# Kernel tuning notes

Hardware: AMD Instinct MI355X
Metric: run time of the kernel (lower is better)

## Reference

```python
import jax, jax.numpy as jnp
import numpy as np

B, M, S = 4, 1024, 1024
D, H, FF = 1024, 16, 4096
NE, P = 128, 1
HD = D // H
EPS = 1e-5


def _layer_norm(x, g, b):
    mu = x.mean(-1, keepdims=True)
    var = ((x - mu) ** 2).mean(-1, keepdims=True)
    return (x - mu) * jax.lax.rsqrt(var + EPS) * g + b


def _mha(q_in, kv_in, in_w, in_b, out_w, out_b):
    # torch nn.MultiheadAttention: packed in_proj_weight [3D, D], y = x @ W.T + b
    wq, wk, wv = in_w[:D], in_w[D:2 * D], in_w[2 * D:]
    bq, bk, bv = in_b[:D], in_b[D:2 * D], in_b[2 * D:]
    q = (q_in @ wq.T + bq).reshape(q_in.shape[0], q_in.shape[1], H, HD)
    k = (kv_in @ wk.T + bk).reshape(kv_in.shape[0], kv_in.shape[1], H, HD)
    v = (kv_in @ wv.T + bv).reshape(kv_in.shape[0], kv_in.shape[1], H, HD)
    scores = jnp.einsum('bqhd,bkhd->bhqk', q, k) / jnp.sqrt(jnp.float32(HD))
    attn = jax.nn.softmax(scores, axis=-1)
    o = jnp.einsum('bhqk,bkhd->bqhd', attn, v).reshape(q_in.shape[0], q_in.shape[1], D)
    return o @ out_w.T + out_b


def _soft_moe(h, phi, exp_w, exp_b):
    # h: [b, m, FF]; phi: [FF, n, p]
    logits = jnp.einsum('bmd,dnp->bmnp', h, phi)
    dispatch = jax.nn.softmax(logits, axis=1)  # over tokens m
    b, m, n, p = logits.shape
    combine = jax.nn.softmax(logits.reshape(b, m, n * p), axis=-1).reshape(b, m, n, p)
    slots = jnp.einsum('bmd,bmnp->bnpd', h, dispatch)  # [b, n, p, FF]
    y = jnp.einsum('bnpd,ndo->bnpo', slots, exp_w) + exp_b[None, :, None, :]  # [b, n, p, D]
    return jnp.einsum('bnpo,bmnp->bmo', y, combine)


def setup_inputs() -> dict:
    key = jax.random.key(0)
    ks = jax.random.split(key, 16)
    sc = 0.02

    def rn(k, shape):
        return jax.random.normal(k, shape, jnp.float32) * sc

    return {
        'tgt': jax.random.normal(ks[0], (B, M, D), jnp.float32),
        'memory': jax.random.normal(ks[1], (B, S, D), jnp.float32),
        'sa_in_w': rn(ks[2], (3 * D, D)), 'sa_in_b': jnp.zeros((3 * D,), jnp.float32),
        'sa_out_w': rn(ks[3], (D, D)), 'sa_out_b': jnp.zeros((D,), jnp.float32),
        'ca_in_w': rn(ks[4], (3 * D, D)), 'ca_in_b': jnp.zeros((3 * D,), jnp.float32),
        'ca_out_w': rn(ks[5], (D, D)), 'ca_out_b': jnp.zeros((D,), jnp.float32),
        'norm1_g': jnp.ones((D,), jnp.float32), 'norm1_b': jnp.zeros((D,), jnp.float32),
        'norm2_g': jnp.ones((D,), jnp.float32), 'norm2_b': jnp.zeros((D,), jnp.float32),
        'norm3_g': jnp.ones((D,), jnp.float32), 'norm3_b': jnp.zeros((D,), jnp.float32),
        'lin_w': rn(ks[6], (FF, D)), 'lin_b': jnp.zeros((FF,), jnp.float32),
        'phi': rn(ks[7], (FF, NE, P)),
        'exp_w': rn(ks[8], (NE, FF, D)), 'exp_b': jnp.zeros((NE, D), jnp.float32),
    }


def reference(tgt, memory, sa_in_w, sa_in_b, sa_out_w, sa_out_b,
              ca_in_w, ca_in_b, ca_out_w, ca_out_b,
              norm1_g, norm1_b, norm2_g, norm2_b, norm3_g, norm3_b,
              lin_w, lin_b, phi, exp_w, exp_b):
    # post-norm (norm_first=False), dropout=0 (eval)
    x = tgt
    x = _layer_norm(x + _mha(x, x, sa_in_w, sa_in_b, sa_out_w, sa_out_b), norm1_g, norm1_b)
    x = _layer_norm(x + _mha(x, memory, ca_in_w, ca_in_b, ca_out_w, ca_out_b), norm2_g, norm2_b)
    h = jax.nn.relu(x @ lin_w.T + lin_b)  # [B, M, FF]
    ff = _soft_moe(h, phi, exp_w, exp_b)  # [B, M, D]
    x = _layer_norm(x + ff, norm3_g, norm3_b)
    return x
```

## Files before the change

kernel.cpp:

```cpp
#include <hip/hip_runtime.h>
#include <cstdint>
#include <cstddef>

typedef unsigned short u16;
typedef unsigned int   u32;
typedef short bf16x8 __attribute__((ext_vector_type(8)));
typedef float f32x4  __attribute__((ext_vector_type(4)));
typedef u16   u16x8  __attribute__((ext_vector_type(8)));
typedef u16   u16x4  __attribute__((ext_vector_type(4)));
typedef u16   u16x2  __attribute__((ext_vector_type(2)));

constexpr int B_  = 4;
constexpr int M_  = 1024;
constexpr int S_  = 1024;
constexpr int D_  = 1024;
constexpr int H_  = 16;
constexpr int FF_ = 4096;
constexpr int NE_ = 128;

__device__ __forceinline__ u16 f2bf(float f) {
    u32 u = __builtin_bit_cast(u32, f);
    u = (u + 0x7fffu + ((u >> 16) & 1u)) >> 16;
    return (u16)u;
}
__device__ __forceinline__ float bf2f(u16 u) {
    u32 x = ((u32)u) << 16;
    return __builtin_bit_cast(float, x);
}
__device__ __forceinline__ void gload_lds16(const u16* g, u16* l) {
    __builtin_amdgcn_global_load_lds(
        (const __attribute__((address_space(1))) u32*)g,
        (__attribute__((address_space(3))) u32*)l, 16, 0, 0);
}

template<int RELU>
__global__ __launch_bounds__(512, 1) void gemm256_mfma(
    const u16* __restrict__ A, const u16* __restrict__ W,
    const float* __restrict__ bias, u16* __restrict__ C,
    int K, int N, int lda, int ldw)
{
    __shared__ u16 lds[49152];
    const int tid = threadIdx.x;
    const int w = tid >> 6, l = tid & 63;
    const int wr = w >> 2, wc = w & 3;
    const int fr = l & 15, g = l >> 4;
    const int bm = blockIdx.y * 256, bn = blockIdx.x * 256;

    const int qcol = (((l & 3) ^ ((l >> 3) & 3))) * 8;
    const int srow = w * 16 + (l >> 2);
    const u16* aG0 = A + (size_t)(bm + srow) * lda + qcol;
    const u16* aG1 = aG0 + (size_t)128 * lda;
    const u16* bG0 = W + (size_t)(bn + srow) * ldw + qcol;
    const u16* bG1 = bG0 + (size_t)128 * ldw;
    const int wofs = w * 512;

    const int qsw = (g ^ ((fr >> 1) & 3)) * 8;
    const int aoff = (wr * 128 + fr) * 32 + qsw;
    const int boff = (wc * 64 + fr) * 32 + qsw;

    f32x4 acc[8][4];
#pragma unroll
    for (int i = 0; i < 8; ++i)
#pragma unroll
        for (int j = 0; j < 4; ++j)
#pragma unroll
            for (int q = 0; q < 4; ++q) acc[i][j][q] = 0.f;

    gload_lds16(aG0, &lds[0 + wofs]);
    gload_lds16(aG1, &lds[4096 + wofs]);
    gload_lds16(bG0, &lds[24576 + wofs]);
    gload_lds16(bG1, &lds[24576 + 4096 + wofs]);
    aG0 += 32; aG1 += 32; bG0 += 32; bG1 += 32;
    gload_lds16(aG0, &lds[8192 + wofs]);
    gload_lds16(aG1, &lds[8192 + 4096 + wofs]);
    gload_lds16(bG0, &lds[32768 + wofs]);
    gload_lds16(bG1, &lds[32768 + 4096 + wofs]);
    aG0 += 32; aG1 += 32; bG0 += 32; bG1 += 32;
    asm volatile("s_waitcnt vmcnt(4)" ::: "memory");
    __builtin_amdgcn_s_barrier();
    __builtin_amdgcn_sched_barrier(0);

    int rb = 0;

#define G256_STEP(ISSUE_, VMOPT_)                                            \
  {                                                                          \
    const int wb_ = (rb >= 1) ? rb - 1 : 2;                                  \
    const u16* Ab_ = &lds[rb * 8192];                                        \
    const u16* Bb_ = &lds[24576 + rb * 8192];                                \
    u16* Aw_ = &lds[wb_ * 8192];                                             \
    u16* Bw_ = &lds[24576 + wb_ * 8192];                                     \
    bf16x8 af_[4], bf_[4];                                                   \
    _Pragma("unroll") for (int mf = 0; mf < 4; ++mf)                         \
      af_[mf] = *(const bf16x8*)(Ab_ + aoff + mf * 512);                     \
    _Pragma("unroll") for (int nf = 0; nf < 4; ++nf)                         \
      bf_[nf] = *(const bf16x8*)(Bb_ + boff + nf * 512);                     \
    if (ISSUE_) {                                                            \
      gload_lds16(aG0, Aw_ + wofs);                                          \
      gload_lds16(aG1, Aw_ + 4096 + wofs);                                   \
    }                                                                        \
    __builtin_amdgcn_s_barrier();                                            \
    __builtin_amdgcn_sched_barrier(0);                                       \
    __builtin_amdgcn_s_setprio(1);                                           \
    _Pragma("unroll") for (int mf = 0; mf < 4; ++mf)                         \
      _Pragma("unroll") for (int nf = 0; nf < 4; ++nf)                       \
        acc[mf][nf] = __builtin_amdgcn_mfma_f32_16x16x32_bf16(               \
            af_[mf], bf_[nf], acc[mf][nf], 0, 0, 0);                         \
    __builtin_amdgcn_s_setprio(0);                                           \
    __builtin_amdgcn_s_barrier();                                            \
    __builtin_amdgcn_sched_barrier(0);                                       \
    _Pragma("unroll") for (int mf = 0; mf < 4; ++mf)                         \
      af_[mf] = *(const bf16x8*)(Ab_ + aoff + 2048 + mf * 512);              \
    if (ISSUE_) {                                                            \
      gload_lds16(bG0, Bw_ + wofs);                                          \
      gload_lds16(bG1, Bw_ + 4096 + wofs);                                   \
      aG0 += 32; aG1 += 32; bG0 += 32; bG1 += 32;                            \
    }                                                                        \
    VMOPT_                                                                   \
    __builtin_amdgcn_s_barrier();                                            \
    __builtin_amdgcn_sched_barrier(0);                                       \
    __builtin_amdgcn_s_setprio(1);                                           \
    _Pragma("unroll") for (int mf = 0; mf < 4; ++mf)                         \
      _Pragma("unroll") for (int nf = 0; nf < 4; ++nf)                       \
        acc[mf + 4][nf] = __builtin_amdgcn_mfma_f32_16x16x32_bf16(           \
            af_[mf], bf_[nf], acc[mf + 4][nf], 0, 0, 0);                     \
    __builtin_amdgcn_s_setprio(0);                                           \
    __builtin_amdgcn_s_barrier();                                            \
    __builtin_amdgcn_sched_barrier(0);                                       \
    rb = (rb == 2) ? 0 : rb + 1;                                             \
  }

    const int nstep = K >> 5;
    for (int t = 0; t < nstep - 2; ++t) {
        G256_STEP(1, asm volatile("s_waitcnt vmcnt(4)" ::: "memory");)
    }
    G256_STEP(0, asm volatile("s_waitcnt vmcnt(0)" ::: "memory");)
    G256_STEP(0, )
#undef G256_STEP

    const int row0 = bm + wr * 128 + g * 4;
    const int col0 = bn + wc * 64 + fr;
#pragma unroll
    for (int nf = 0; nf < 4; ++nf) {
        const int col = col0 + nf * 16;
        const float bv = bias[col];
#pragma unroll
        for (int mf = 0; mf < 8; ++mf) {
#pragma unroll
            for (int j = 0; j < 4; ++j) {
                float v = acc[mf][nf][j] + bv;
                if (RELU) v = fmaxf(v, 0.f);
                C[(size_t)(row0 + mf * 16 + j) * N + col] = f2bf(v);
            }
        }
    }
}

template<int OUT_BF16, int RELU, int HAS_BIAS>
__global__ __launch_bounds__(256) void gemm_bt_mfma(
    const u16* __restrict__ A, const u16* __restrict__ W,
    const float* __restrict__ bias, void* __restrict__ Cout,
    int K, int N, int lda, int ldw,
    size_t sA, size_t sW, size_t sC)
{
    __shared__ u16 As[128 * 32];
    __shared__ u16 Bs[128 * 32];
    const int tid = threadIdx.x;
    const int w = tid >> 6, l = tid & 63;
    const int bm = blockIdx.y * 128, bn = blockIdx.x * 128;
    const u16* Ab = A + (size_t)blockIdx.z * sA;
    const u16* Wb = W + (size_t)blockIdx.z * sW;

    const int wr = w >> 1, wc = w & 1;
    const int sr = l >> 2;
    const int sk = (l & 3) * 8;
    const u16* aG0 = Ab + (size_t)(bm + w * 16 + sr) * lda + sk;
    const u16* aG1 = Ab + (size_t)(bm + (w + 4) * 16 + sr) * lda + sk;
    const u16* bG0 = Wb + (size_t)(bn + w * 16 + sr) * ldw + sk;
    const u16* bG1 = Wb + (size_t)(bn + (w + 4) * 16 + sr) * ldw + sk;
    u16* aL0 = &As[w * 512];
    u16* aL1 = &As[(w + 4) * 512];
    u16* bL0 = &Bs[w * 512];
    u16* bL1 = &Bs[(w + 4) * 512];

    const int fr = l & 15;
    const int fk = (l >> 4) * 8;

    f32x4 acc[4][4];
#pragma unroll
    for (int i = 0; i < 4; ++i)
#pragma unroll
        for (int j = 0; j < 4; ++j)
#pragma unroll
            for (int q = 0; q < 4; ++q) acc[i][j][q] = 0.f;

    for (int k0 = 0; k0 < K; k0 += 32) {
        __syncthreads();
        gload_lds16(aG0, aL0);
        gload_lds16(aG1, aL1);
        gload_lds16(bG0, bL0);
        gload_lds16(bG1, bL1);
        aG0 += 32; aG1 += 32; bG0 += 32; bG1 += 32;
        __syncthreads();
        bf16x8 af[4], bfr[4];
#pragma unroll
        for (int m = 0; m < 4; ++m)
            af[m] = *(const bf16x8*)&As[(wr * 64 + m * 16 + fr) * 32 + fk];
#pragma unroll
        for (int n = 0; n < 4; ++n)
            bfr[n] = *(const bf16x8*)&Bs[(wc * 64 + n * 16 + fr) * 32 + fk];
#pragma unroll
        for (int m = 0; m < 4; ++m)
#pragma unroll
            for (int n = 0; n < 4; ++n)
                acc[m][n] = __builtin_amdgcn_mfma_f32_16x16x32_bf16(
                    af[m], bfr[n], acc[m][n], 0, 0, 0);
    }

    const int row0 = bm + wr * 64 + (l >> 4) * 4;
    const int col0 = bn + wc * 64;
#pragma unroll
    for (int n = 0; n < 4; ++n) {
        const int col = col0 + n * 16 + fr;
        float bv = 0.f;
        if (HAS_BIAS) bv = bias[col];
#pragma unroll
        for (int m = 0; m < 4; ++m) {
            const int row = row0 + m * 16;
#pragma unroll
            for (int j = 0; j < 4; ++j) {
                float v = acc[m][n][j] + bv;
                if (RELU) v = fmaxf(v, 0.f);
                const size_t idx = (size_t)blockIdx.z * sC + (size_t)(row + j) * N + col;
                if (OUT_BF16) ((u16*)Cout)[idx] = f2bf(v);
                else          ((float*)Cout)[idx] = v;
            }
        }
    }
}

__global__ __launch_bounds__(256) void flash_attn_kernel(
    const u16* __restrict__ Q, int qs,
    const u16* __restrict__ K, int ks,
    const u16* __restrict__ V, int vs,
    u16* __restrict__ O, int Slen)
{
    __shared__ u16 Qs[64][72];
    __shared__ u16 Ks[64][72];
    __shared__ u16 Vt[64][72];
    __shared__ u16 Pw[4][16][72];
    const int b = blockIdx.z, hh = blockIdx.y;
    const int m0 = blockIdx.x * 64;
    const int tid = threadIdx.x;
    const int w = tid >> 6, l = tid & 63;
    const int lq = l & 15, g = l >> 4;

    {
        const int row = tid >> 2, cg = (tid & 3) * 16;
        const u16* qp = Q + ((size_t)b * M_ + m0 + row) * qs + hh * 64 + cg;
        u16x8 v0 = *(const u16x8*)qp;
        u16x8 v1 = *(const u16x8*)(qp + 8);
        u16x8 o0, o1;
#pragma unroll
        for (int i = 0; i < 8; ++i) {
            o0[i] = f2bf(bf2f(v0[i]) * 0.125f);
            o1[i] = f2bf(bf2f(v1[i]) * 0.125f);
        }
        *(u16x8*)&Qs[row][cg]     = o0;
        *(u16x8*)&Qs[row][cg + 8] = o1;
    }
    __syncthreads();
    bf16x8 qf[2];
    qf[0] = *(const bf16x8*)&Qs[w * 16 + lq][g * 8];
    qf[1] = *(const bf16x8*)&Qs[w * 16 + lq][32 + g * 8];

    f32x4 acc_o[4];
#pragma unroll
    for (int nb = 0; nb < 4; ++nb)
#pragma unroll
        for (int j = 0; j < 4; ++j) acc_o[nb][j] = 0.f;
    float m_run = -1e30f, l_run = 0.f;

    const int kp = tid & 31, dg = tid >> 5;
    const int krow = tid >> 2, kcg = (tid & 3) * 16;

    for (int s0 = 0; s0 < Slen; s0 += 64) {
        __syncthreads();
        {
            const u16* kpp = K + ((size_t)b * Slen + s0 + krow) * ks + hh * 64 + kcg;
            *(u16x8*)&Ks[krow][kcg]     = *(const u16x8*)kpp;
            *(u16x8*)&Ks[krow][kcg + 8] = *(const u16x8*)(kpp + 8);
        }
        {
            const u16* vp0 = V + ((size_t)b * Slen + s0 + 2 * kp) * vs + hh * 64 + dg * 8;
            const u16* vp1 = vp0 + vs;
            u16x8 a = *(const u16x8*)vp0;
            u16x8 c = *(const u16x8*)vp1;
#pragma unroll
            for (int i = 0; i < 8; ++i) {
                u16x2 pk; pk[0] = a[i]; pk[1] = c[i];
                *(u16x2*)&Vt[dg * 8 + i][2 * kp] = pk;
            }
        }
        __syncthreads();

        f32x4 s4[4];
#pragma unroll
        for (int mb = 0; mb < 4; ++mb) {
            f32x4 z = {0.f, 0.f, 0.f, 0.f};
            bf16x8 a0 = *(const bf16x8*)&Ks[mb * 16 + lq][g * 8];
            bf16x8 a1 = *(const bf16x8*)&Ks[mb * 16 + lq][32 + g * 8];
            z = __builtin_amdgcn_mfma_f32_16x16x32_bf16(a0, qf[0], z, 0, 0, 0);
            z = __builtin_amdgcn_mfma_f32_16x16x32_bf16(a1, qf[1], z, 0, 0, 0);
            s4[mb] = z;
        }

        float pm = -1e30f;
#pragma unroll
        for (int mb = 0; mb < 4; ++mb)
#pragma unroll
            for (int j = 0; j < 4; ++j) pm = fmaxf(pm, s4[mb][j]);
        pm = fmaxf(pm, __shfl_xor(pm, 16));
        pm = fmaxf(pm, __shfl_xor(pm, 32));

        u16 pbf[4][4];
        float ls = 0.f;
        if (__all(pm - m_run <= 8.f)) {
#pragma unroll
            for (int mb = 0; mb < 4; ++mb)
#pragma unroll
                for (int j = 0; j < 4; ++j) {
                    float p = __expf(s4[mb][j] - m_run);
                    ls += p;
                    pbf[mb][j] = f2bf(p);
                }
            ls += __shfl_xor(ls, 16);
            ls += __shfl_xor(ls, 32);
            l_run += ls;
        } else {
            const float m_new = fmaxf(m_run, pm);
            const float alpha = __expf(m_run - m_new);
#pragma unroll
            for (int mb = 0; mb < 4; ++mb)
#pragma unroll
                for (int j = 0; j < 4; ++j) {
                    float p = __expf(s4[mb][j] - m_new);
                    ls += p;
                    pbf[mb][j] = f2bf(p);
                }
            ls += __shfl_xor(ls, 16);
            ls += __shfl_xor(ls, 32);
            l_run = l_run * alpha + ls;
            m_run = m_new;
            float al[4];
#pragma unroll
            for (int j = 0; j < 4; ++j) al[j] = __shfl(alpha, 4 * g + j);
#pragma unroll
            for (int nb = 0; nb < 4; ++nb)
#pragma unroll
                for (int j = 0; j < 4; ++j) acc_o[nb][j] *= al[j];
        }

#pragma unroll
        for (int mb = 0; mb < 4; ++mb) {
            u16x4 pk;
            pk[0] = pbf[mb][0]; pk[1] = pbf[mb][1];
            pk[2] = pbf[mb][2]; pk[3] = pbf[mb][3];
            *(u16x4*)&Pw[w][lq][mb * 16 + g * 4] = pk;
        }

#pragma unroll
        for (int kc = 0; kc < 2; ++kc) {
            bf16x8 pa = *(const bf16x8*)&Pw[w][lq][kc * 32 + g * 8];
#pragma unroll
            for (int nb = 0; nb < 4; ++nb) {
                bf16x8 bv = *(const bf16x8*)&Vt[nb * 16 + lq][kc * 32 + g * 8];
                acc_o[nb] = __builtin_amdgcn_mfma_f32_16x16x32_bf16(pa, bv, acc_o[nb], 0, 0, 0);
            }
        }
    }

    float linv[4];
#pragma unroll
    for (int j = 0; j < 4; ++j) linv[j] = 1.f / __shfl(l_run, 4 * g + j);
#pragma unroll
    for (int nb = 0; nb < 4; ++nb)
#pragma unroll
        for (int j = 0; j < 4; ++j) {
            const size_t row = (size_t)b * M_ + m0 + w * 16 + 4 * g + j;
            O[row * D_ + hh * 64 + nb * 16 + lq] = f2bf(acc_o[nb][j] * linv[j]);
        }
}

__global__ __launch_bounds__(256) void cvt_multi_kernel(
    const float* __restrict__ s0, u16* __restrict__ d0,
    const float* __restrict__ s1, u16* __restrict__ d1,
    const float* __restrict__ s2, u16* __restrict__ d2,
    const float* __restrict__ s3, u16* __restrict__ d3,
    const float* __restrict__ s4, u16* __restrict__ d4,
    const float* __restrict__ s5, u16* __restrict__ d5,
    const float* __restrict__ s6, u16* __restrict__ d6)
{
    int blk = blockIdx.x;
    const float* s; u16* d;
    if      (blk < 2048) { s = s0; d = d0; }
    else if (blk < 4096) { s = s1; d = d1; blk -= 2048; }
    else if (blk < 5632) { s = s2; d = d2; blk -= 4096; }
    else if (blk < 6144) { s = s3; d = d3; blk -= 5632; }
    else if (blk < 7680) { s = s4; d = d4; blk -= 6144; }
    else if (blk < 8192) { s = s5; d = d5; blk -= 7680; }
    else                 { s = s6; d = d6; blk -= 8192; }
    const size_t i = ((size_t)blk * 256 + threadIdx.x) * 8;
    float4 a = *(const float4*)(s + i);
    float4 b = *(const float4*)(s + i + 4);
    u16x8 o;
    o[0] = f2bf(a.x); o[1] = f2bf(a.y); o[2] = f2bf(a.z); o[3] = f2bf(a.w);
    o[4] = f2bf(b.x); o[5] = f2bf(b.y); o[6] = f2bf(b.z); o[7] = f2bf(b.w);
    *(u16x8*)(d + i) = o;
}

__global__ __launch_bounds__(256) void transpose_f32_bf16_kernel(
    const float* __restrict__ src, u16* __restrict__ dst, int R, int C,
    size_t sI, size_t sO)
{
    __shared__ u16 t[32][33];
    src += (size_t)blockIdx.z * sI;
    dst += (size_t)blockIdx.z * sO;
    const int c0 = blockIdx.x * 32, r0 = blockIdx.y * 32;
    const int x = threadIdx.x & 31, y = threadIdx.x >> 5;
    for (int i = y; i < 32; i += 8)
        t[i][x] = f2bf(src[(size_t)(r0 + i) * C + c0 + x]);
    __syncthreads();
    for (int i = y; i < 32; i += 8)
        dst[(size_t)(c0 + i) * R + r0 + x] = t[x][i];
}

__global__ __launch_bounds__(256) void transpose_bf16_kernel(
    const u16* __restrict__ src, u16* __restrict__ dst, int R, int C,
    size_t sI, size_t sO)
{
    __shared__ u16 t[32][33];
    src += (size_t)blockIdx.z * sI;
    dst += (size_t)blockIdx.z * sO;
    const int c0 = blockIdx.x * 32, r0 = blockIdx.y * 32;
    const int x = threadIdx.x & 31, y = threadIdx.x >> 5;
    for (int i = y; i < 32; i += 8)
        t[i][x] = src[(size_t)(r0 + i) * C + c0 + x];
    __syncthreads();
    for (int i = y; i < 32; i += 8)
        dst[(size_t)(c0 + i) * R + r0 + x] = t[x][i];
}

__global__ __launch_bounds__(256) void resid_ln_kernel(
    const float* __restrict__ X, const float* __restrict__ R,
    const float* __restrict__ g, const float* __restrict__ bt,
    float* __restrict__ Y, u16* __restrict__ Ybf)
{
    __shared__ float s1[4], s2[4];
    const size_t row = blockIdx.x;
    const int tid = threadIdx.x;
    const float4 x4 = *(const float4*)(X + row * 1024 + tid * 4);
    const float4 r4 = *(const float4*)(R + row * 1024 + tid * 4);
    float v[4] = {x4.x + r4.x, x4.y + r4.y, x4.z + r4.z, x4.w + r4.w};
    float s = v[0] + v[1] + v[2] + v[3];
    float q = v[0] * v[0] + v[1] * v[1] + v[2] * v[2] + v[3] * v[3];
#pragma unroll
    for (int off = 32; off; off >>= 1) {
        s += __shfl_xor(s, off);
        q += __shfl_xor(q, off);
    }
    if ((tid & 63) == 0) { s1[tid >> 6] = s; s2[tid >> 6] = q; }
    __syncthreads();
    s = s1[0] + s1[1] + s1[2] + s1[3];
    q = s2[0] + s2[1] + s2[2] + s2[3];
    const float mu = s * (1.f / 1024.f);
    const float var = q * (1.f / 1024.f) - mu * mu;
    const float rinv = rsqrtf(var + 1e-5f);
    const float4 g4 = *(const float4*)(g + tid * 4);
    const float4 b4 = *(const float4*)(bt + tid * 4);
    float o[4];
    o[0] = (v[0] - mu) * rinv * g4.x + b4.x;
    o[1] = (v[1] - mu) * rinv * g4.y + b4.y;
    o[2] = (v[2] - mu) * rinv * g4.z + b4.z;
    o[3] = (v[3] - mu) * rinv * g4.w + b4.w;
    *(float4*)(Y + row * 1024 + tid * 4) = *(float4*)o;
    if (Ybf) {
        u16x4 ob;
        ob[0] = f2bf(o[0]); ob[1] = f2bf(o[1]);
        ob[2] = f2bf(o[2]); ob[3] = f2bf(o[3]);
        *(u16x4*)(Ybf + row * 1024 + tid * 4) = ob;
    }
}

__global__ __launch_bounds__(256) void dispatch_softmax_T_kernel(
    const float* __restrict__ logitsP, u16* __restrict__ dispT)
{
    __shared__ float red[4];
    constexpr size_t CH = (size_t)B_ * M_ * NE_;
    const int n = blockIdx.x, b = blockIdx.y;
    u16* O = dispT + ((size_t)b * NE_ + n) * M_;
    const int tid = threadIdx.x;
    float v[4];
#pragma unroll
    for (int i = 0; i < 4; ++i) {
        const size_t idx = (size_t)(b * M_ + tid + 256 * i) * NE_ + n;
        v[i] = logitsP[idx] + logitsP[CH + idx] + logitsP[2 * CH + idx] + logitsP[3 * CH + idx];
    }
    float mx = fmaxf(fmaxf(v[0], v[1]), fmaxf(v[2], v[3]));
#pragma unroll
    for (int off = 32; off; off >>= 1) mx = fmaxf(mx, __shfl_xor(mx, off));
    if ((tid & 63) == 0) red[tid >> 6] = mx;
    __syncthreads();
    mx = fmaxf(fmaxf(red[0], red[1]), fmaxf(red[2], red[3]));
    __syncthreads();
    float e[4], s = 0.f;
#pragma unroll
    for (int i = 0; i < 4; ++i) { e[i] = __expf(v[i] - mx); s += e[i]; }
#pragma unroll
    for (int off = 32; off; off >>= 1) s += __shfl_xor(s, off);
    if ((tid & 63) == 0) red[tid >> 6] = s;
    __syncthreads();
    s = red[0] + red[1] + red[2] + red[3];
    const float inv = 1.f / s;
#pragma unroll
    for (int i = 0; i < 4; ++i) O[tid + 256 * i] = f2bf(e[i] * inv);
}

__global__ __launch_bounds__(64) void combine_softmax_kernel(
    const float* __restrict__ logitsP, u16* __restrict__ comb)
{
    constexpr size_t CH = (size_t)B_ * M_ * NE_;
    const size_t row = blockIdx.x;
    const int lane = threadIdx.x;
    const size_t i0 = row * NE_ + lane;
    const size_t i1 = i0 + 64;
    float a = logitsP[i0] + logitsP[CH + i0] + logitsP[2 * CH + i0] + logitsP[3 * CH + i0];
    float c = logitsP[i1] + logitsP[CH + i1] + logitsP[2 * CH + i1] + logitsP[3 * CH + i1];
    float mx = fmaxf(a, c);
#pragma unroll
    for (int off = 32; off; off >>= 1) mx = fmaxf(mx, __shfl_xor(mx, off));
    float e0 = __expf(a - mx), e1 = __expf(c - mx);
    float s = e0 + e1;
#pragma unroll
    for (int off = 32; off; off >>= 1) s += __shfl_xor(s, off);
    const float inv = 1.f / s;
    comb[row * NE_ + lane]      = f2bf(e0 * inv);
    comb[row * NE_ + lane + 64] = f2bf(e1 * inv);
}

__global__ __launch_bounds__(256) void expert_partial_kernel(
    const float* __restrict__ slots, const float* __restrict__ exp_w,
    float* __restrict__ part)
{
    __shared__ float sl[4][512];
    const int n = blockIdx.x;
    const int c = blockIdx.y;
    const int f0 = c * 512;
    const int t = threadIdx.x;
    for (int i = t; i < 2048; i += 256) {
        const int b = i >> 9, f = i & 511;
        sl[b][f] = slots[((size_t)b * NE_ + n) * FF_ + f0 + f];
    }
    __syncthreads();
    const int d4 = t * 4;
    const float* wp = exp_w + ((size_t)n * FF_ + f0) * D_ + d4;
    f32x4 acc[4];
#pragma unroll
    for (int b = 0; b < 4; ++b)
#pragma unroll
        for (int j = 0; j < 4; ++j) acc[b][j] = 0.f;
#pragma unroll 4
    for (int f = 0; f < 512; ++f) {
        const float4 w4 = *(const float4*)wp;
        wp += D_;
#pragma unroll
        for (int b = 0; b < 4; ++b) {
            const float s = sl[b][f];
            acc[b][0] = fmaf(s, w4.x, acc[b][0]);
            acc[b][1] = fmaf(s, w4.y, acc[b][1]);
            acc[b][2] = fmaf(s, w4.z, acc[b][2]);
            acc[b][3] = fmaf(s, w4.w, acc[b][3]);
        }
    }
#pragma unroll
    for (int b = 0; b < 4; ++b)
        *(f32x4*)&part[(((size_t)c * 4 + b) * NE_ + n) * D_ + d4] = acc[b];
}

__global__ __launch_bounds__(256) void reduce_yT_kernel(
    const float* __restrict__ part, const float* __restrict__ exp_b,
    u16* __restrict__ yT)
{
    __shared__ float tile[32][33];
    const int d0 = blockIdx.x * 32, n0 = blockIdx.y * 32, b = blockIdx.z;
    const int x = threadIdx.x & 31, y = threadIdx.x >> 5;
    for (int i = y; i < 32; i += 8) {
        const int n = n0 + i;
        float s = exp_b[(size_t)n * D_ + d0 + x];
#pragma unroll
        for (int c = 0; c < 8; ++c)
            s += part[(((size_t)c * 4 + b) * NE_ + n) * D_ + d0 + x];
        tile[i][x] = s;
    }
    __syncthreads();
    for (int i = y; i < 32; i += 8)
        yT[((size_t)b * D_ + d0 + i) * NE_ + n0 + x] = f2bf(tile[x][i]);
}

extern "C" void kernel_launch(void* const* d_in, const int* in_sizes, int n_in,
                              void* d_out, int out_size, void* d_ws, size_t ws_size,
                              hipStream_t stream)
{
    const float* tgt      = (const float*)d_in[0];
    const float* memry    = (const float*)d_in[1];
    const float* sa_in_w  = (const float*)d_in[2];
    const float* sa_in_b  = (const float*)d_in[3];
    const float* sa_out_w = (const float*)d_in[4];
    const float* sa_out_b = (const float*)d_in[5];
    const float* ca_in_w  = (const float*)d_in[6];
    const float* ca_in_b  = (const float*)d_in[7];
    const float* ca_out_w = (const float*)d_in[8];
    const float* ca_out_b = (const float*)d_in[9];
    const float* norm1_g  = (const float*)d_in[10];
    const float* norm1_b  = (const float*)d_in[11];
    const float* norm2_g  = (const float*)d_in[12];
    const float* norm2_b  = (const float*)d_in[13];
    const float* norm3_g  = (const float*)d_in[14];
    const float* norm3_b  = (const float*)d_in[15];
    const float* lin_w    = (const float*)d_in[16];
    const float* lin_b    = (const float*)d_in[17];
    const float* phi      = (const float*)d_in[18];
    const float* exp_w    = (const float*)d_in[19];
    const float* exp_b    = (const float*)d_in[20];

    float* ws = (float*)d_ws;
    u16*   qkv_bf  = (u16*)(ws);
    float* proj    = ws + 6291456;
    float* x1      = ws + 10485760;
    float* x2      = ws + 14680064;
    float* logitsP = ws + 18874368;
    float* part    = ws + 20971520;
    u16*   h_bf    = (u16*)(ws + 25165824);
    u16*   hT_bf   = (u16*)(ws + 33554432);
    u16*   obuf_bf = (u16*)(ws + 41943040);
    u16*   x1_bf   = (u16*)(ws + 44040192);
    u16*   x2_bf   = (u16*)(ws + 46137344);
    u16*   tgt_bf  = (u16*)(ws + 48234496);
    u16*   mem_bf  = (u16*)(ws + 50331648);
    u16*   dispT   = (u16*)(ws + 52428800);
    u16*   comb_bf = (u16*)(ws + 52690944);
    u16*   yT_bf   = (u16*)(ws + 52953088);
    float* slots   = ws + 53215232;
    u16*   w_sa_in = (u16*)(ws + 55312384);
    u16*   w_sa_out= (u16*)(ws + 56885248);
    u16*   w_ca_in = (u16*)(ws + 57409536);
    u16*   w_ca_out= (u16*)(ws + 58982400);
    u16*   w_lin   = (u16*)(ws + 59506688);
    u16*   phiT    = (u16*)(ws + 61603840);

    cvt_multi_kernel<<<10240, 256, 0, stream>>>(
        tgt, tgt_bf, memry, mem_bf, sa_in_w, w_sa_in, sa_out_w, w_sa_out,
        ca_in_w, w_ca_in, ca_out_w, w_ca_out, lin_w, w_lin);
    transpose_f32_bf16_kernel<<<dim3(4, 128, 1), 256, 0, stream>>>(phi, phiT, 4096, 128, 0, 0);

    gemm256_mfma<0><<<dim3(12, 16, 1), 512, 0, stream>>>(
        tgt_bf, w_sa_in, sa_in_b, qkv_bf, 1024, 3072, 1024, 1024);
    flash_attn_kernel<<<dim3(16, 16, 4), 256, 0, stream>>>(
        qkv_bf, 3072, qkv_bf + 1024, 3072, qkv_bf + 2048, 3072, obuf_bf, S_);
    gemm_bt_mfma<0, 0, 1><<<dim3(8, 32, 1), 256, 0, stream>>>(
        obuf_bf, w_sa_out, sa_out_b, proj, 1024, 1024, 1024, 1024, 0, 0, 0);
    resid_ln_kernel<<<4096, 256, 0, stream>>>(tgt, proj, norm1_g, norm1_b, x1, x1_bf);

    u16* qca_bf = qkv_bf;
    u16* kvca_bf = qkv_bf + (size_t)4096 * 1024;
    gemm_bt_mfma<1, 0, 1><<<dim3(8, 32, 1), 256, 0, stream>>>(
        x1_bf, w_ca_in, ca_in_b, qca_bf, 1024, 1024, 1024, 1024, 0, 0, 0);
    gemm256_mfma<0><<<dim3(8, 16, 1), 512, 0, stream>>>(
        mem_bf, w_ca_in + (size_t)1024 * 1024, ca_in_b + 1024,
        kvca_bf, 1024, 2048, 1024, 1024);
    flash_attn_kernel<<<dim3(16, 16, 4), 256, 0, stream>>>(
        qca_bf, 1024, kvca_bf, 2048, kvca_bf + 1024, 2048, obuf_bf, S_);
    gemm_bt_mfma<0, 0, 1><<<dim3(8, 32, 1), 256, 0, stream>>>(
        obuf_bf, w_ca_out, ca_out_b, proj, 1024, 1024, 1024, 1024, 0, 0, 0);
    resid_ln_kernel<<<4096, 256, 0, stream>>>(x1, proj, norm2_g, norm2_b, x2, x2_bf);

    gemm256_mfma<1><<<dim3(16, 16, 1), 512, 0, stream>>>(
        x2_bf, w_lin, lin_b, h_bf, 1024, 4096, 1024, 1024);
    gemm_bt_mfma<0, 0, 0><<<dim3(1, 32, 4), 256, 0, stream>>>(
        h_bf, phiT, nullptr, logitsP, 1024, 128, 4096, 4096,
        1024, 1024, (size_t)B_ * M_ * NE_);
    dispatch_softmax_T_kernel<<<dim3(NE_, B_), 256, 0, stream>>>(logitsP, dispT);
    combine_softmax_kernel<<<dim3(B_ * M_), 64, 0, stream>>>(logitsP, comb_bf);
    transpose_bf16_kernel<<<dim3(128, 32, 4), 256, 0, stream>>>(
        h_bf, hT_bf, 1024, 4096, (size_t)M_ * FF_, (size_t)M_ * FF_);
    gemm_bt_mfma<0, 0, 0><<<dim3(32, 1, 4), 256, 0, stream>>>(
        dispT, hT_bf, nullptr, slots, 1024, 4096, 1024, 1024,
        (size_t)NE_ * M_, (size_t)FF_ * M_, (size_t)NE_ * FF_);
    expert_partial_kernel<<<dim3(NE_, 8), 256, 0, stream>>>(slots, exp_w, part);
    reduce_yT_kernel<<<dim3(32, 4, 4), 256, 0, stream>>>(part, exp_b, yT_bf);
    gemm_bt_mfma<0, 0, 0><<<dim3(8, 8, 4), 256, 0, stream>>>(
        comb_bf, yT_bf, nullptr, proj, 128, 1024, 128, 128,
        (size_t)M_ * NE_, (size_t)D_ * NE_, (size_t)M_ * D_);
    resid_ln_kernel<<<4096, 256, 0, stream>>>(x2, proj, norm3_g, norm3_b,
                                              (float*)d_out, nullptr);
}
```

Measured before the change: 832.0 us.

## Fuse hT transpose into FFN GEMM epilogue and double-buffer flash attention K/V

The FFN up-projection GEMM now also writes the transposed activation hT straight from its epilogue in packed 4-element stores, so the separate bf16 transpose kernel is no longer needed. That removes one extra read and write of a 32 MB tensor and one launch, at the cost of scattered 8-byte stores in the epilogue. Flash attention now loads Q fragments straight from global memory into registers, dropping the Q LDS staging and its barrier. It also double-buffers the K/V LDS tiles, prefetching the next tile into registers while computing on the current one, which costs more LDS and registers.

```diff
diff --git a/kernel.cpp b/kernel.cpp
--- a/kernel.cpp
+++ b/kernel.cpp
@@ -33,10 +33,11 @@
         (__attribute__((address_space(3))) u32*)l, 16, 0, 0);
 }
 
-template<int RELU>
+template<int RELU, int WRITE_HT>
 __global__ __launch_bounds__(512, 1) void gemm256_mfma(
     const u16* __restrict__ A, const u16* __restrict__ W,
     const float* __restrict__ bias, u16* __restrict__ C,
+    u16* __restrict__ HT,
     int K, int N, int lda, int ldw)
 {
     __shared__ u16 lds[49152];
@@ -145,11 +146,18 @@
         const float bv = bias[col];
 #pragma unroll
         for (int mf = 0; mf < 8; ++mf) {
+            const int rowm = row0 + mf * 16;
+            u16 o[4];
 #pragma unroll
             for (int j = 0; j < 4; ++j) {
                 float v = acc[mf][nf][j] + bv;
                 if (RELU) v = fmaxf(v, 0.f);
-                C[(size_t)(row0 + mf * 16 + j) * N + col] = f2bf(v);
+                o[j] = f2bf(v);
+                C[(size_t)(rowm + j) * N + col] = o[j];
+            }
+            if (WRITE_HT) {
+                u16x4 pk; pk[0] = o[0]; pk[1] = o[1]; pk[2] = o[2]; pk[3] = o[3];
+                *(u16x4*)&HT[(((size_t)(rowm >> 10)) * N + col) * 1024 + (rowm & 1023)] = pk;
             }
         }
     }
@@ -244,9 +252,8 @@
     const u16* __restrict__ V, int vs,
     u16* __restrict__ O, int Slen)
 {
-    __shared__ u16 Qs[64][72];
-    __shared__ u16 Ks[64][72];
-    __shared__ u16 Vt[64][72];
+    __shared__ u16 Ks[2][64][72];
+    __shared__ u16 Vt[2][64][72];
     __shared__ u16 Pw[4][16][72];
     const int b = blockIdx.z, hh = blockIdx.y;
     const int m0 = blockIdx.x * 64;
@@ -254,24 +261,20 @@
     const int w = tid >> 6, l = tid & 63;
     const int lq = l & 15, g = l >> 4;
 
+    bf16x8 qf[2];
     {
-        const int row = tid >> 2, cg = (tid & 3) * 16;
-        const u16* qp = Q + ((size_t)b * M_ + m0 + row) * qs + hh * 64 + cg;
-        u16x8 v0 = *(const u16x8*)qp;
-        u16x8 v1 = *(const u16x8*)(qp + 8);
+        const u16* qp = Q + ((size_t)b * M_ + m0 + w * 16 + lq) * qs + hh * 64;
+        u16x8 v0 = *(const u16x8*)(qp + g * 8);
+        u16x8 v1 = *(const u16x8*)(qp + 32 + g * 8);
         u16x8 o0, o1;
 #pragma unroll
         for (int i = 0; i < 8; ++i) {
             o0[i] = f2bf(bf2f(v0[i]) * 0.125f);
             o1[i] = f2bf(bf2f(v1[i]) * 0.125f);
         }
-        *(u16x8*)&Qs[row][cg]     = o0;
-        *(u16x8*)&Qs[row][cg + 8] = o1;
-    }
-    __syncthreads();
-    bf16x8 qf[2];
-    qf[0] = *(const bf16x8*)&Qs[w * 16 + lq][g * 8];
-    qf[1] = *(const bf16x8*)&Qs[w * 16 + lq][32 + g * 8];
+        qf[0] = __builtin_bit_cast(bf16x8, o0);
+        qf[1] = __builtin_bit_cast(bf16x8, o1);
+    }
 
     f32x4 acc_o[4];
 #pragma unroll
@@ -283,32 +286,42 @@
     const int kp = tid & 31, dg = tid >> 5;
     const int krow = tid >> 2, kcg = (tid & 3) * 16;
 
-    for (int s0 = 0; s0 < Slen; s0 += 64) {
-        __syncthreads();
-        {
-            const u16* kpp = K + ((size_t)b * Slen + s0 + krow) * ks + hh * 64 + kcg;
-            *(u16x8*)&Ks[krow][kcg]     = *(const u16x8*)kpp;
-            *(u16x8*)&Ks[krow][kcg + 8] = *(const u16x8*)(kpp + 8);
-        }
-        {
-            const u16* vp0 = V + ((size_t)b * Slen + s0 + 2 * kp) * vs + hh * 64 + dg * 8;
-            const u16* vp1 = vp0 + vs;
-            u16x8 a = *(const u16x8*)vp0;
-            u16x8 c = *(const u16x8*)vp1;
-#pragma unroll
-            for (int i = 0; i < 8; ++i) {
-                u16x2 pk; pk[0] = a[i]; pk[1] = c[i];
-                *(u16x2*)&Vt[dg * 8 + i][2 * kp] = pk;
-            }
-        }
-        __syncthreads();
+    const int nt = Slen >> 6;
+    u16x8 kv0, kv1, va, vb;
+
+#define ATT_LOAD(T_)                                                          \
+    {                                                                         \
+        const u16* kpp = K + ((size_t)b * Slen + (T_) * 64 + krow) * ks + hh * 64 + kcg; \
+        kv0 = *(const u16x8*)kpp;                                             \
+        kv1 = *(const u16x8*)(kpp + 8);                                       \
+        const u16* vp0 = V + ((size_t)b * Slen + (T_) * 64 + 2 * kp) * vs + hh * 64 + dg * 8; \
+        va = *(const u16x8*)vp0;                                              \
+        vb = *(const u16x8*)(vp0 + vs);                                       \
+    }
+#define ATT_WRITE(BUF_)                                                       \
+    {                                                                         \
+        *(u16x8*)&Ks[BUF_][krow][kcg]     = kv0;                              \
+        *(u16x8*)&Ks[BUF_][krow][kcg + 8] = kv1;                              \
+        _Pragma("unroll") for (int i = 0; i < 8; ++i) {                       \
+            u16x2 pk; pk[0] = va[i]; pk[1] = vb[i];                           \
+            *(u16x2*)&Vt[BUF_][dg * 8 + i][2 * kp] = pk;                      \
+        }                                                                     \
+    }
+
+    ATT_LOAD(0)
+    ATT_WRITE(0)
+    __syncthreads();
+
+    for (int t = 0; t < nt; ++t) {
+        if (t + 1 < nt) ATT_LOAD(t + 1)
+        const int cb = t & 1;
 
         f32x4 s4[4];
 #pragma unroll
         for (int mb = 0; mb < 4; ++mb) {
             f32x4 z = {0.f, 0.f, 0.f, 0.f};
-            bf16x8 a0 = *(const bf16x8*)&Ks[mb * 16 + lq][g * 8];
-            bf16x8 a1 = *(const bf16x8*)&Ks[mb * 16 + lq][32 + g * 8];
+            bf16x8 a0 = *(const bf16x8*)&Ks[cb][mb * 16 + lq][g * 8];
+            bf16x8 a1 = *(const bf16x8*)&Ks[cb][mb * 16 + lq][32 + g * 8];
             z = __builtin_amdgcn_mfma_f32_16x16x32_bf16(a0, qf[0], z, 0, 0, 0);
             z = __builtin_amdgcn_mfma_f32_16x16x32_bf16(a1, qf[1], z, 0, 0, 0);
             s4[mb] = z;
@@ -373,11 +386,16 @@
             bf16x8 pa = *(const bf16x8*)&Pw[w][lq][kc * 32 + g * 8];
 #pragma unroll
             for (int nb = 0; nb < 4; ++nb) {
-                bf16x8 bv = *(const bf16x8*)&Vt[nb * 16 + lq][kc * 32 + g * 8];
+                bf16x8 bv = *(const bf16x8*)&Vt[cb][nb * 16 + lq][kc * 32 + g * 8];
                 acc_o[nb] = __builtin_amdgcn_mfma_f32_16x16x32_bf16(pa, bv, acc_o[nb], 0, 0, 0);
             }
         }
-    }
+
+        if (t + 1 < nt) ATT_WRITE((t + 1) & 1)
+        __syncthreads();
+    }
+#undef ATT_LOAD
+#undef ATT_WRITE
 
     float linv[4];
 #pragma unroll
@@ -429,22 +447,6 @@
     const int x = threadIdx.x & 31, y = threadIdx.x >> 5;
     for (int i = y; i < 32; i += 8)
         t[i][x] = f2bf(src[(size_t)(r0 + i) * C + c0 + x]);
-    __syncthreads();
-    for (int i = y; i < 32; i += 8)
-        dst[(size_t)(c0 + i) * R + r0 + x] = t[x][i];
-}
-
-__global__ __launch_bounds__(256) void transpose_bf16_kernel(
-    const u16* __restrict__ src, u16* __restrict__ dst, int R, int C,
-    size_t sI, size_t sO)
-{
-    __shared__ u16 t[32][33];
-    src += (size_t)blockIdx.z * sI;
-    dst += (size_t)blockIdx.z * sO;
-    const int c0 = blockIdx.x * 32, r0 = blockIdx.y * 32;
-    const int x = threadIdx.x & 31, y = threadIdx.x >> 5;
-    for (int i = y; i < 32; i += 8)
-        t[i][x] = src[(size_t)(r0 + i) * C + c0 + x];
     __syncthreads();
     for (int i = y; i < 32; i += 8)
         dst[(size_t)(c0 + i) * R + r0 + x] = t[x][i];
@@ -662,8 +664,8 @@
         ca_in_w, w_ca_in, ca_out_w, w_ca_out, lin_w, w_lin);
     transpose_f32_bf16_kernel<<<dim3(4, 128, 1), 256, 0, stream>>>(phi, phiT, 4096, 128, 0, 0);
 
-    gemm256_mfma<0><<<dim3(12, 16, 1), 512, 0, stream>>>(
-        tgt_bf, w_sa_in, sa_in_b, qkv_bf, 1024, 3072, 1024, 1024);
+    gemm256_mfma<0, 0><<<dim3(12, 16, 1), 512, 0, stream>>>(
+        tgt_bf, w_sa_in, sa_in_b, qkv_bf, nullptr, 1024, 3072, 1024, 1024);
     flash_attn_kernel<<<dim3(16, 16, 4), 256, 0, stream>>>(
         qkv_bf, 3072, qkv_bf + 1024, 3072, qkv_bf + 2048, 3072, obuf_bf, S_);
     gemm_bt_mfma<0, 0, 1><<<dim3(8, 32, 1), 256, 0, stream>>>(
@@ -674,24 +676,22 @@
     u16* kvca_bf = qkv_bf + (size_t)4096 * 1024;
     gemm_bt_mfma<1, 0, 1><<<dim3(8, 32, 1), 256, 0, stream>>>(
         x1_bf, w_ca_in, ca_in_b, qca_bf, 1024, 1024, 1024, 1024, 0, 0, 0);
-    gemm256_mfma<0><<<dim3(8, 16, 1), 512, 0, stream>>>(
+    gemm256_mfma<0, 0><<<dim3(8, 16, 1), 512, 0, stream>>>(
         mem_bf, w_ca_in + (size_t)1024 * 1024, ca_in_b + 1024,
-        kvca_bf, 1024, 2048, 1024, 1024);
+        kvca_bf, nullptr, 1024, 2048, 1024, 1024);
     flash_attn_kernel<<<dim3(16, 16, 4), 256, 0, stream>>>(
         qca_bf, 1024, kvca_bf, 2048, kvca_bf + 1024, 2048, obuf_bf, S_);
     gemm_bt_mfma<0, 0, 1><<<dim3(8, 32, 1), 256, 0, stream>>>(
         obuf_bf, w_ca_out, ca_out_b, proj, 1024, 1024, 1024, 1024, 0, 0, 0);
     resid_ln_kernel<<<4096, 256, 0, stream>>>(x1, proj, norm2_g, norm2_b, x2, x2_bf);
 
-    gemm256_mfma<1><<<dim3(16, 16, 1), 512, 0, stream>>>(
-        x2_bf, w_lin, lin_b, h_bf, 1024, 4096, 1024, 1024);
+    gemm256_mfma<1, 1><<<dim3(16, 16, 1), 512, 0, stream>>>(
+        x2_bf, w_lin, lin_b, h_bf, hT_bf, 1024, 4096, 1024, 1024);
     gemm_bt_mfma<0, 0, 0><<<dim3(1, 32, 4), 256, 0, stream>>>(
         h_bf, phiT, nullptr, logitsP, 1024, 128, 4096, 4096,
         1024, 1024, (size_t)B_ * M_ * NE_);
     dispatch_softmax_T_kernel<<<dim3(NE_, B_), 256, 0, stream>>>(logitsP, dispT);
     combine_softmax_kernel<<<dim3(B_ * M_), 64, 0, stream>>>(logitsP, comb_bf);
-    transpose_bf16_kernel<<<dim3(128, 32, 4), 256, 0, stream>>>(
-        h_bf, hT_bf, 1024, 4096, (size_t)M_ * FF_, (size_t)M_ * FF_);
     gemm_bt_mfma<0, 0, 0><<<dim3(32, 1, 4), 256, 0, stream>>>(
         dispT, hT_bf, nullptr, slots, 1024, 4096, 1024, 1024,
         (size_t)NE_ * M_, (size_t)FF_ * M_, (size_t)NE_ * FF_);
```

After: 831.8 us. Within noise of the previous version (-0.0%).
